# Performance work log

Measured on AMD Instinct MI355X. Metric: run time of the kernel, lower is better.

Reference implementation:

```python
import jax, jax.numpy as jnp
import numpy as np

HIDDEN = 64
HALF = 32
VOCAB = 64
B, L = 256, 2048


def _l2norm(x):
    # matches torch F.normalize(dim=-1, eps=1e-12)
    return x / jnp.maximum(jnp.linalg.norm(x, axis=-1, keepdims=True), 1e-12)


def setup_inputs() -> dict:
    key = jax.random.key(0)
    ks = jax.random.split(key, 16)
    s = 0.02
    return {
        "seq": jax.random.randint(ks[0], (B, L), 0, VOCAB),
        "embed": jax.random.normal(ks[1], (VOCAB, HIDDEN), jnp.float32) * s,
        "W1": jax.random.normal(ks[2], (2 * HIDDEN, HIDDEN), jnp.float32) * s,
        "b1": jnp.zeros((2 * HIDDEN,), jnp.float32),
        "W2": jax.random.normal(ks[3], (HIDDEN, 2 * HIDDEN), jnp.float32) * s,
        "b2": jnp.zeros((HIDDEN,), jnp.float32),
        "ln_g": jnp.ones((HIDDEN,), jnp.float32),
        "ln_b": jnp.zeros((HIDDEN,), jnp.float32),
        "Ws": jax.random.normal(ks[4], (HALF, HIDDEN), jnp.float32) * s,
        "bs": jnp.zeros((HALF,), jnp.float32),
        "We": jax.random.normal(ks[5], (HALF, HIDDEN), jnp.float32) * s,
        "be": jnp.zeros((HALF,), jnp.float32),
        "Wrp": jax.random.normal(ks[6], (HIDDEN, 2 * HALF), jnp.float32) * s,
        "brp": jnp.zeros((HIDDEN,), jnp.float32),
        "Wo": jax.random.normal(ks[7], (VOCAB, HIDDEN), jnp.float32) * s,
        "bo": jnp.zeros((VOCAB,), jnp.float32),
    }


def reference(seq, embed, W1, b1, W2, b2, ln_g, ln_b, Ws, bs, We, be, Wrp, brp, Wo, bo):
    # Encoder: embed -> LayerNorm(h + FF(h))
    h0 = embed[seq]                                     # [B,L,H]
    ff = jnp.maximum(h0 @ W1.T + b1, 0.0) @ W2.T + b2
    x = h0 + ff
    mu = x.mean(-1, keepdims=True)
    var = x.var(-1, keepdims=True)
    h = (x - mu) / jnp.sqrt(var + 1e-5) * ln_g + ln_b   # [B,L,H]

    Bn, Ln, _ = h.shape
    half = Ws.shape[0]
    hs_all = h @ Ws.T + bs                              # [B,L,half]
    he_all = h @ We.T + be

    # sequential delta-rule memory writes over t = 0 .. L-2
    hs_seq = jnp.swapaxes(hs_all[:, :-1], 0, 1)         # [L-1,B,half]
    he_seq = jnp.swapaxes(he_all[:, :-1], 0, 1)
    scales = (jnp.arange(1, Ln) / Ln).astype(h.dtype)   # (t+1)/L
    M0 = jnp.zeros((Bn, half, half), h.dtype)

    def step(carry, inp):
        M_s, M_e = carry
        hs, he, sc = inp
        ks_ = _l2norm(hs)
        ke_ = _l2norm(he)
        vps = jnp.einsum('bij,bj->bi', M_s, ks_)
        vpe = jnp.einsum('bij,bj->bi', M_e, ke_)
        M_s = M_s + (hs - vps)[:, :, None] * ks_[:, None, :]
        M_e = M_e + sc * (he - vpe)[:, :, None] * ke_[:, None, :]
        return (M_s, M_e), None

    (M_s, M_e), _ = jax.lax.scan(step, (M0, M0), (hs_seq, he_seq, scales))

    # read with last-position query
    qs = _l2norm(hs_all[:, -1])
    qe = _l2norm(he_all[:, -1])
    rs = jnp.einsum('bij,bj->bi', M_s, qs)
    re = jnp.einsum('bij,bj->bi', M_e, qe)
    r = jnp.concatenate([rs, re], axis=-1)              # [B, 2*half]
    return (r @ Wrp.T + brp) @ Wo.T + bo                # [B, vocab]
```

## Files before the change

kernel.cpp:

```cpp
#include <hip/hip_runtime.h>

#define HIDDEN 64
#define HALFD  32
#define VOCAB  64
#define BATCH  256
#define SEQLEN 2048

#define RLF(v, sl) __int_as_float(__builtin_amdgcn_readlane(__float_as_int(v), (sl)))
#define RLI(v, sl) __builtin_amdgcn_readlane((v), (sl))
#define GIX(j,m) (((j)==0?0:(j)==1?7:(j)==2?13:(j)==3?18:(j)==4?22:(j)==5?25:27) + (m) - (j) - 1)
#define OM(m) (((m)*((m)+1))>>1)

__global__ __launch_bounds__(64) void vocab_kernel(
    const float* __restrict__ embed, const float* __restrict__ W1, const float* __restrict__ b1,
    const float* __restrict__ W2, const float* __restrict__ b2,
    const float* __restrict__ ln_g, const float* __restrict__ ln_b,
    const float* __restrict__ Ws, const float* __restrict__ bs,
    const float* __restrict__ We, const float* __restrict__ be,
    float* __restrict__ ws)
{
    const int v = blockIdx.x;
    const int tid = threadIdx.x;

    __shared__ float e_s[64];
    __shared__ float a1_s[128];
    __shared__ float h_s[64];

    e_s[tid] = embed[v * 64 + tid];
    __syncthreads();

    float acc0 = b1[tid], acc1 = b1[tid + 64];
    #pragma unroll 8
    for (int m = 0; m < 64; ++m) {
        float ev = e_s[m];
        acc0 = fmaf(ev, W1[tid * 64 + m], acc0);
        acc1 = fmaf(ev, W1[(tid + 64) * 64 + m], acc1);
    }
    a1_s[tid]      = fmaxf(acc0, 0.0f);
    a1_s[tid + 64] = fmaxf(acc1, 0.0f);
    __syncthreads();

    float ff = b2[tid];
    #pragma unroll 8
    for (int m = 0; m < 128; ++m) ff = fmaf(a1_s[m], W2[tid * 128 + m], ff);
    float x = e_s[tid] + ff;

    float s = x, s2 = x * x;
    #pragma unroll
    for (int off = 32; off >= 1; off >>= 1) {
        s  += __shfl_xor(s,  off, 64);
        s2 += __shfl_xor(s2, off, 64);
    }
    float mu  = s * (1.0f / 64.0f);
    float var = s2 * (1.0f / 64.0f) - mu * mu;
    float hval = (x - mu) * rsqrtf(var + 1e-5f) * ln_g[tid] + ln_b[tid];
    h_s[tid] = hval;
    __syncthreads();

    const int j = tid & 31;
    const bool is_s = tid < 32;
    const float* W = is_s ? Ws : We;
    float acc = is_s ? bs[j] : be[j];
    #pragma unroll 8
    for (int m = 0; m < 64; ++m) acc = fmaf(h_s[m], W[j * 64 + m], acc);

    float n2 = acc * acc;
    #pragma unroll
    for (int off = 16; off >= 1; off >>= 1) n2 += __shfl_xor(n2, off, 64);
    float norm = sqrtf(n2);
    float kn = acc / fmaxf(norm, 1e-12f);

    const int base = v * 32 + j;
    if (is_s) { ws[base]        = kn; ws[4096 + base] = acc; }
    else      { ws[2048 + base] = kn; ws[6144 + base] = acc; }
}

__global__ __launch_bounds__(256) void gram_kernel(float* __restrict__ ws)
{
    const int w = blockIdx.x;
    const int tid = threadIdx.x;
    __shared__ float k_s[2048];
    const float* kb = ws + w * 2048;
    for (int i = tid; i < 2048; i += 256) k_s[i] = kb[i];
    __syncthreads();
    const int a  = tid >> 2;
    const int b0 = (tid & 3) << 4;
    float* Gw = ws + 8192 + w * 4096 + a * 64;
    for (int bb = 0; bb < 16; ++bb) {
        const int bcol = b0 + bb;
        float acc = 0.f;
        #pragma unroll
        for (int m = 0; m < 32; ++m) acc = fmaf(k_s[a * 32 + m], k_s[bcol * 32 + m], acc);
        Gw[bcol] = acc;
    }
}

struct Chunk {
    int   tokv;
    int   tk[8];
    float grow[8];
    float W[36];
};

__global__ __launch_bounds__(128) void scan_kernel(
    const int* __restrict__ seq, const float* __restrict__ ws,
    const float* __restrict__ Wrp, const float* __restrict__ brp,
    const float* __restrict__ Wo, const float* __restrict__ bo,
    float* __restrict__ out)
{
    const int b    = blockIdx.x;
    const int tid  = threadIdx.x;
    const int w    = tid >> 6;
    const int lane = tid & 63;
    const int l7   = lane & 7;
    const bool is_e = (w == 1);

    __shared__ __align__(16) float Wtab[2 * 256 * 36];
    __shared__ __align__(16) int   toklds[SEQLEN];
    __shared__ float wacc_s[2][64];
    __shared__ float r_s[64];
    __shared__ float t1_s[64];

    const float* Gg     = ws + 8192 + w * 4096;
    float*       Wtab_w = Wtab + w * (256 * 36);

    {
        const int4* sq4 = (const int4*)(seq + b * SEQLEN);
        int4* tl = (int4*)toklds;
        #pragma unroll
        for (int i = 0; i < 4; ++i) tl[tid + i * 128] = sq4[tid + i * 128];
    }
    __syncthreads();

    {
        const float invL = 1.0f / (float)SEQLEN;
        #pragma unroll
        for (int qq = 0; qq < 4; ++qq) {
            const int c = lane + (qq << 6);
            int tj[8];
            #pragma unroll
            for (int j = 0; j < 8; ++j) tj[j] = toklds[c * 8 + j];

            float f[8];
            float fb = (float)(8 * c + 1) * invL;
            #pragma unroll
            for (int j = 0; j < 8; ++j) f[j] = is_e ? (fb + (float)j * invL) : 1.0f;
            if (c == 255) f[7] = 0.0f;

            float g[28];
            #pragma unroll
            for (int j = 0; j < 7; ++j)
                #pragma unroll
                for (int m = j + 1; m < 8; ++m) g[GIX(j, m)] = Gg[tj[j] * 64 + tj[m]];

            float Wp[36];
            #pragma unroll
            for (int m = 0; m < 8; ++m) {
                float col[8];
                col[m] = f[m];
                #pragma unroll
                for (int j = 6; j >= 0; --j) {
                    if (j < m) {
                        float acc = 0.0f;
                        #pragma unroll
                        for (int p = 1; p < 8; ++p)
                            if (p > j && p <= m) acc = fmaf(g[GIX(j, p)], col[p], acc);
                        col[j] = -f[j] * acc;
                    }
                }
                #pragma unroll
                for (int j = 0; j < 8; ++j)
                    if (j <= m) Wp[OM(m) + j] = col[j];
            }

            float4* dst = (float4*)&Wtab_w[c * 36];
            #pragma unroll
            for (int i = 0; i < 9; ++i)
                dst[i] = make_float4(Wp[4*i], Wp[4*i+1], Wp[4*i+2], Wp[4*i+3]);
        }
    }
    __syncthreads();

    Chunk A, B;
    float u, waccv = 0.0f;

    A.tokv = toklds[2040 + l7];
    #pragma unroll
    for (int j = 0; j < 8; ++j) A.tk[j] = RLI(A.tokv, j);
    #pragma unroll
    for (int j = 0; j < 8; ++j) A.grow[j] = Gg[A.tk[j] * 64 + lane];
    {
        const float4* wsrc = (const float4*)&Wtab_w[255 * 36];
        #pragma unroll
        for (int i = 0; i < 9; ++i) {
            float4 v = wsrc[i];
            A.W[4*i] = v.x; A.W[4*i+1] = v.y; A.W[4*i+2] = v.z; A.W[4*i+3] = v.w;
        }
    }
    B.tokv = toklds[2032 + l7];
    u = Gg[A.tk[7] * 64 + lane];

    auto body = [&](Chunk& cur, Chunk& nxt, int c) {
        float bp = __shfl(u, cur.tokv, 64);

        const int cm1 = (c > 0) ? c - 1 : 0;
        const int cm2 = (c > 1) ? c - 2 : 0;
        #pragma unroll
        for (int j = 0; j < 8; ++j) nxt.tk[j] = RLI(nxt.tokv, j);
        #pragma unroll
        for (int j = 0; j < 8; ++j) nxt.grow[j] = Gg[nxt.tk[j] * 64 + lane];
        {
            const float4* wsrc = (const float4*)&Wtab_w[cm1 * 36];
            #pragma unroll
            for (int i = 0; i < 9; ++i) {
                float4 v = wsrc[i];
                nxt.W[4*i] = v.x; nxt.W[4*i+1] = v.y; nxt.W[4*i+2] = v.z; nxt.W[4*i+3] = v.w;
            }
        }
        int tokv2 = toklds[cm2 * 8 + l7];

        float t0 = RLF(bp, 0), t1 = RLF(bp, 1), t2 = RLF(bp, 2), t3 = RLF(bp, 3);
        float t4 = RLF(bp, 4), t5 = RLF(bp, 5), t6 = RLF(bp, 6), t7 = RLF(bp, 7);

        const float* W = cur.W;
        float s7 = W[35] * t7;
        float s6 = fmaf(W[27], t6, W[34] * t7);
        float s5 = fmaf(W[20], t5, W[26] * t6) + W[33] * t7;
        float s4 = fmaf(W[14], t4, W[19] * t5) + fmaf(W[25], t6, W[32] * t7);
        float s3 = fmaf(W[9],  t3, W[13] * t4) + fmaf(W[18], t5, fmaf(W[24], t6, W[31] * t7));
        float s2 = fmaf(W[5],  t2, W[8]  * t3) + fmaf(W[12], t4, W[17] * t5) + fmaf(W[23], t6, W[30] * t7);
        float s1 = fmaf(W[2],  t1, W[4]  * t2) + fmaf(W[7],  t3, W[11] * t4) + fmaf(W[16], t5, fmaf(W[22], t6, W[29] * t7));
        float s0 = fmaf(W[0],  t0, W[1]  * t1) + fmaf(W[3],  t2, W[6]  * t3) + fmaf(W[10], t4, W[15] * t5) + fmaf(W[21], t6, W[28] * t7);

        float dA = fmaf(cur.grow[0], s0, fmaf(cur.grow[1], s1, fmaf(cur.grow[2], s2, cur.grow[3] * s3)));
        float dB = fmaf(cur.grow[4], s4, fmaf(cur.grow[5], s5, fmaf(cur.grow[6], s6, cur.grow[7] * s7)));
        u -= (dA + dB);

        waccv += (lane == cur.tk[0]) ? s0 : 0.0f;
        waccv += (lane == cur.tk[1]) ? s1 : 0.0f;
        waccv += (lane == cur.tk[2]) ? s2 : 0.0f;
        waccv += (lane == cur.tk[3]) ? s3 : 0.0f;
        waccv += (lane == cur.tk[4]) ? s4 : 0.0f;
        waccv += (lane == cur.tk[5]) ? s5 : 0.0f;
        waccv += (lane == cur.tk[6]) ? s6 : 0.0f;
        waccv += (lane == cur.tk[7]) ? s7 : 0.0f;

        cur.tokv = tokv2;
    };

    for (int c = 255; c >= 1; c -= 2) {
        body(A, B, c);
        body(B, A, c - 1);
    }

    wacc_s[w][lane] = waccv;
    __syncthreads();

    if (tid < 64) {
        const int w2  = tid >> 5;
        const int rho = tid & 31;
        const float* vv = ws + 4096 + w2 * 2048;
        const float* wa = &wacc_s[w2][0];
        float acc = 0.0f;
        #pragma unroll 8
        for (int tok = 0; tok < 64; ++tok) acc = fmaf(wa[tok], vv[tok * 32 + rho], acc);
        r_s[tid] = acc;
    }
    __syncthreads();

    if (tid < 64) {
        float acc = brp[tid];
        #pragma unroll 8
        for (int m = 0; m < 64; ++m) acc = fmaf(Wrp[tid * 64 + m], r_s[m], acc);
        t1_s[tid] = acc;
    }
    __syncthreads();
    if (tid < 64) {
        float acc = bo[tid];
        #pragma unroll 8
        for (int m = 0; m < 64; ++m) acc = fmaf(Wo[tid * 64 + m], t1_s[m], acc);
        out[b * 64 + tid] = acc;
    }
}

extern "C" void kernel_launch(void* const* d_in, const int* in_sizes, int n_in,
                              void* d_out, int out_size, void* d_ws, size_t ws_size,
                              hipStream_t stream)
{
    const int*   seq   = (const int*)  d_in[0];
    const float* embed = (const float*)d_in[1];
    const float* W1    = (const float*)d_in[2];
    const float* b1    = (const float*)d_in[3];
    const float* W2    = (const float*)d_in[4];
    const float* b2    = (const float*)d_in[5];
    const float* ln_g  = (const float*)d_in[6];
    const float* ln_b  = (const float*)d_in[7];
    const float* Ws    = (const float*)d_in[8];
    const float* bs    = (const float*)d_in[9];
    const float* We    = (const float*)d_in[10];
    const float* be    = (const float*)d_in[11];
    const float* Wrp   = (const float*)d_in[12];
    const float* brp   = (const float*)d_in[13];
    const float* Wo    = (const float*)d_in[14];
    const float* bo    = (const float*)d_in[15];
    float* ws  = (float*)d_ws;
    float* out = (float*)d_out;

    hipLaunchKernelGGL(vocab_kernel, dim3(VOCAB), dim3(64), 0, stream,
                       embed, W1, b1, W2, b2, ln_g, ln_b, Ws, bs, We, be, ws);
    hipLaunchKernelGGL(gram_kernel, dim3(2), dim3(256), 0, stream, ws);
    hipLaunchKernelGGL(scan_kernel, dim3(BATCH), dim3(128), 0, stream,
                       seq, ws, Wrp, brp, Wo, bo, out);
}
```

Measured before the change: 211.1 us.

## Stage per-chunk W packs in global workspace instead of LDS when space allows

Adds a scan kernel variant that writes the per-chunk triangular W coefficients to a padded global workspace region and reads tokens straight from global memory, dropping the large LDS tables. The old LDS path is kept as a fallback when the workspace is too small. The aim is to cut LDS use and raise occupancy or lower LDS pressure, at the cost of extra global and L2 traffic on the serial scan's critical path.

New measurement: 254.3 us. 1.2x slower.

```diff
diff --git a/kernel.cpp b/kernel.cpp
--- a/kernel.cpp
+++ b/kernel.cpp
@@ -5,6 +5,9 @@
 #define VOCAB  64
 #define BATCH  256
 #define SEQLEN 2048
+
+#define WOFF    16384
+#define WSTRIDE 40
 
 #define RLF(v, sl) __int_as_float(__builtin_amdgcn_readlane(__float_as_int(v), (sl)))
 #define RLI(v, sl) __builtin_amdgcn_readlane((v), (sl))
@@ -95,6 +98,41 @@
     }
 }
 
+static __device__ __forceinline__ void build_wpack(
+    const int* tj, float fb, float invL, bool is_e, bool is_last, float* Wp,
+    const float* __restrict__ Gg)
+{
+    float f[8];
+    #pragma unroll
+    for (int j = 0; j < 8; ++j) f[j] = is_e ? (fb + (float)j * invL) : 1.0f;
+    if (is_last) f[7] = 0.0f;
+
+    float g[28];
+    #pragma unroll
+    for (int j = 0; j < 7; ++j)
+        #pragma unroll
+        for (int m = j + 1; m < 8; ++m) g[GIX(j, m)] = Gg[tj[j] * 64 + tj[m]];
+
+    #pragma unroll
+    for (int m = 0; m < 8; ++m) {
+        float col[8];
+        col[m] = f[m];
+        #pragma unroll
+        for (int j = 6; j >= 0; --j) {
+            if (j < m) {
+                float acc = 0.0f;
+                #pragma unroll
+                for (int p = 1; p < 8; ++p)
+                    if (p > j && p <= m) acc = fmaf(g[GIX(j, p)], col[p], acc);
+                col[j] = -f[j] * acc;
+            }
+        }
+        #pragma unroll
+        for (int j = 0; j < 8; ++j)
+            if (j <= m) Wp[OM(m) + j] = col[j];
+    }
+}
+
 struct Chunk {
     int   tokv;
     int   tk[8];
@@ -102,8 +140,8 @@
     float W[36];
 };
 
-__global__ __launch_bounds__(128) void scan_kernel(
-    const int* __restrict__ seq, const float* __restrict__ ws,
+__global__ __launch_bounds__(128, 1) void scan_pre_kernel(
+    const int* __restrict__ seq, float* __restrict__ ws,
     const float* __restrict__ Wrp, const float* __restrict__ brp,
     const float* __restrict__ Wo, const float* __restrict__ bo,
     float* __restrict__ out)
@@ -115,6 +153,146 @@
     const int l7   = lane & 7;
     const bool is_e = (w == 1);
 
+    __shared__ float wacc_s[2][64];
+    __shared__ float r_s[64];
+    __shared__ float t1_s[64];
+
+    const float* Gg  = ws + 8192 + w * 4096;
+    float*       wsW = ws + WOFF + ((size_t)(b * 2 + w)) * (256 * WSTRIDE);
+    const int*   sq  = seq + b * SEQLEN;
+
+    const float invL = 1.0f / (float)SEQLEN;
+
+    #pragma unroll
+    for (int qq = 0; qq < 4; ++qq) {
+        const int c = lane + (qq << 6);
+        int tj[8];
+        #pragma unroll
+        for (int j = 0; j < 8; ++j) tj[j] = sq[c * 8 + j];
+        float Wp[36];
+        build_wpack(tj, (float)(8 * c + 1) * invL, invL, is_e, c == 255, Wp, Gg);
+        float4* dst = (float4*)&wsW[c * WSTRIDE];
+        #pragma unroll
+        for (int i = 0; i < 9; ++i)
+            dst[i] = make_float4(Wp[4*i], Wp[4*i+1], Wp[4*i+2], Wp[4*i+3]);
+    }
+    __syncthreads();
+
+    Chunk A, B;
+    float u, waccv = 0.0f;
+
+    A.tokv = sq[2040 + l7];
+    #pragma unroll
+    for (int j = 0; j < 8; ++j) A.tk[j] = RLI(A.tokv, j);
+    #pragma unroll
+    for (int j = 0; j < 8; ++j) A.grow[j] = Gg[A.tk[j] * 64 + lane];
+    {
+        const float4* wsrc = (const float4*)&wsW[255 * WSTRIDE];
+        #pragma unroll
+        for (int i = 0; i < 9; ++i) {
+            float4 v = wsrc[i];
+            A.W[4*i] = v.x; A.W[4*i+1] = v.y; A.W[4*i+2] = v.z; A.W[4*i+3] = v.w;
+        }
+    }
+    B.tokv = sq[2032 + l7];
+    u = Gg[A.tk[7] * 64 + lane];
+
+    auto body = [&](Chunk& cur, Chunk& nxt, int c) {
+        float bp = __shfl(u, cur.tokv, 64);
+
+        const int cm1 = (c > 0) ? c - 1 : 0;
+        const int cm2 = (c > 1) ? c - 2 : 0;
+        #pragma unroll
+        for (int j = 0; j < 8; ++j) nxt.tk[j] = RLI(nxt.tokv, j);
+        #pragma unroll
+        for (int j = 0; j < 8; ++j) nxt.grow[j] = Gg[nxt.tk[j] * 64 + lane];
+        {
+            const float4* wsrc = (const float4*)&wsW[cm1 * WSTRIDE];
+            #pragma unroll
+            for (int i = 0; i < 9; ++i) {
+                float4 v = wsrc[i];
+                nxt.W[4*i] = v.x; nxt.W[4*i+1] = v.y; nxt.W[4*i+2] = v.z; nxt.W[4*i+3] = v.w;
+            }
+        }
+        int tokv2 = sq[cm2 * 8 + l7];
+
+        float t0 = RLF(bp, 0), t1 = RLF(bp, 1), t2 = RLF(bp, 2), t3 = RLF(bp, 3);
+        float t4 = RLF(bp, 4), t5 = RLF(bp, 5), t6 = RLF(bp, 6), t7 = RLF(bp, 7);
+
+        const float* W = cur.W;
+        float s7 = W[35] * t7;
+        float s6 = fmaf(W[27], t6, W[34] * t7);
+        float s5 = fmaf(W[20], t5, W[26] * t6) + W[33] * t7;
+        float s4 = fmaf(W[14], t4, W[19] * t5) + fmaf(W[25], t6, W[32] * t7);
+        float s3 = fmaf(W[9],  t3, W[13] * t4) + fmaf(W[18], t5, fmaf(W[24], t6, W[31] * t7));
+        float s2 = fmaf(W[5],  t2, W[8]  * t3) + fmaf(W[12], t4, W[17] * t5) + fmaf(W[23], t6, W[30] * t7);
+        float s1 = fmaf(W[2],  t1, W[4]  * t2) + fmaf(W[7],  t3, W[11] * t4) + fmaf(W[16], t5, fmaf(W[22], t6, W[29] * t7));
+        float s0 = fmaf(W[0],  t0, W[1]  * t1) + fmaf(W[3],  t2, W[6]  * t3) + fmaf(W[10], t4, W[15] * t5) + fmaf(W[21], t6, W[28] * t7);
+
+        float dA = fmaf(cur.grow[0], s0, fmaf(cur.grow[1], s1, fmaf(cur.grow[2], s2, cur.grow[3] * s3)));
+        float dB = fmaf(cur.grow[4], s4, fmaf(cur.grow[5], s5, fmaf(cur.grow[6], s6, cur.grow[7] * s7)));
+        u -= (dA + dB);
+
+        waccv += (lane == cur.tk[0]) ? s0 : 0.0f;
+        waccv += (lane == cur.tk[1]) ? s1 : 0.0f;
+        waccv += (lane == cur.tk[2]) ? s2 : 0.0f;
+        waccv += (lane == cur.tk[3]) ? s3 : 0.0f;
+        waccv += (lane == cur.tk[4]) ? s4 : 0.0f;
+        waccv += (lane == cur.tk[5]) ? s5 : 0.0f;
+        waccv += (lane == cur.tk[6]) ? s6 : 0.0f;
+        waccv += (lane == cur.tk[7]) ? s7 : 0.0f;
+
+        cur.tokv = tokv2;
+    };
+
+    for (int c = 255; c >= 1; c -= 2) {
+        body(A, B, c);
+        body(B, A, c - 1);
+    }
+
+    wacc_s[w][lane] = waccv;
+    __syncthreads();
+
+    if (tid < 64) {
+        const int w2  = tid >> 5;
+        const int rho = tid & 31;
+        const float* vv = ws + 4096 + w2 * 2048;
+        const float* wa = &wacc_s[w2][0];
+        float acc = 0.0f;
+        #pragma unroll 8
+        for (int tok = 0; tok < 64; ++tok) acc = fmaf(wa[tok], vv[tok * 32 + rho], acc);
+        r_s[tid] = acc;
+    }
+    __syncthreads();
+
+    if (tid < 64) {
+        float acc = brp[tid];
+        #pragma unroll 8
+        for (int m = 0; m < 64; ++m) acc = fmaf(Wrp[tid * 64 + m], r_s[m], acc);
+        t1_s[tid] = acc;
+    }
+    __syncthreads();
+    if (tid < 64) {
+        float acc = bo[tid];
+        #pragma unroll 8
+        for (int m = 0; m < 64; ++m) acc = fmaf(Wo[tid * 64 + m], t1_s[m], acc);
+        out[b * 64 + tid] = acc;
+    }
+}
+
+__global__ __launch_bounds__(128) void scan_lds_kernel(
+    const int* __restrict__ seq, const float* __restrict__ ws,
+    const float* __restrict__ Wrp, const float* __restrict__ brp,
+    const float* __restrict__ Wo, const float* __restrict__ bo,
+    float* __restrict__ out)
+{
+    const int b    = blockIdx.x;
+    const int tid  = threadIdx.x;
+    const int w    = tid >> 6;
+    const int lane = tid & 63;
+    const int l7   = lane & 7;
+    const bool is_e = (w == 1);
+
     __shared__ __align__(16) float Wtab[2 * 256 * 36];
     __shared__ __align__(16) int   toklds[SEQLEN];
     __shared__ float wacc_s[2][64];
@@ -140,39 +318,8 @@
             int tj[8];
             #pragma unroll
             for (int j = 0; j < 8; ++j) tj[j] = toklds[c * 8 + j];
-
-            float f[8];
-            float fb = (float)(8 * c + 1) * invL;
-            #pragma unroll
-            for (int j = 0; j < 8; ++j) f[j] = is_e ? (fb + (float)j * invL) : 1.0f;
-            if (c == 255) f[7] = 0.0f;
-
-            float g[28];
-            #pragma unroll
-            for (int j = 0; j < 7; ++j)
-                #pragma unroll
-                for (int m = j + 1; m < 8; ++m) g[GIX(j, m)] = Gg[tj[j] * 64 + tj[m]];
-
             float Wp[36];
-            #pragma unroll
-            for (int m = 0; m < 8; ++m) {
-                float col[8];
-                col[m] = f[m];
-                #pragma unroll
-                for (int j = 6; j >= 0; --j) {
-                    if (j < m) {
-                        float acc = 0.0f;
-                        #pragma unroll
-                        for (int p = 1; p < 8; ++p)
-                            if (p > j && p <= m) acc = fmaf(g[GIX(j, p)], col[p], acc);
-                        col[j] = -f[j] * acc;
-                    }
-                }
-                #pragma unroll
-                for (int j = 0; j < 8; ++j)
-                    if (j <= m) Wp[OM(m) + j] = col[j];
-            }
-
+            build_wpack(tj, (float)(8 * c + 1) * invL, invL, is_e, c == 255, Wp, Gg);
             float4* dst = (float4*)&Wtab_w[c * 36];
             #pragma unroll
             for (int i = 0; i < 9; ++i)
@@ -202,7 +349,6 @@
 
     auto body = [&](Chunk& cur, Chunk& nxt, int c) {
         float bp = __shfl(u, cur.tokv, 64);
-
         const int cm1 = (c > 0) ? c - 1 : 0;
         const int cm2 = (c > 1) ? c - 2 : 0;
         #pragma unroll
@@ -309,6 +455,13 @@
     hipLaunchKernelGGL(vocab_kernel, dim3(VOCAB), dim3(64), 0, stream,
                        embed, W1, b1, W2, b2, ln_g, ln_b, Ws, bs, We, be, ws);
     hipLaunchKernelGGL(gram_kernel, dim3(2), dim3(256), 0, stream, ws);
-    hipLaunchKernelGGL(scan_kernel, dim3(BATCH), dim3(128), 0, stream,
-                       seq, ws, Wrp, brp, Wo, bo, out);
-}
+
+    const size_t need = (size_t)(WOFF + BATCH * 2 * 256 * WSTRIDE) * sizeof(float);
+    if (ws_size >= need) {
+        hipLaunchKernelGGL(scan_pre_kernel, dim3(BATCH), dim3(128), 0, stream,
+                           seq, ws, Wrp, brp, Wo, bo, out);
+    } else {
+        hipLaunchKernelGGL(scan_lds_kernel, dim3(BATCH), dim3(128), 0, stream,
+                           seq, ws, Wrp, brp, Wo, bo, out);
+    }
+}
```
